# Optimization experiments

Hardware: AMD Instinct MI355X
Metric: run time of the kernel (lower is better)

The kernel has to match this reference:

```python
import jax, jax.numpy as jnp
import numpy as np

B, T, C = 4, 2048, 1024   # batch, seq_len, n_embd
H, D = 16, 64             # num heads, head dim (H*D == C)


def setup_inputs() -> dict:
    key = jax.random.key(0)
    ks = jax.random.split(key, 6)
    scale = 0.02
    x = jax.random.normal(ks[0], (B, T, C), dtype=jnp.float32)
    Wq = jax.random.normal(ks[1], (H, C, D), dtype=jnp.float32) * scale
    Wk = jax.random.normal(ks[2], (H, C, D), dtype=jnp.float32) * scale
    Wv = jax.random.normal(ks[3], (H, C, D), dtype=jnp.float32) * scale
    Wp = jax.random.normal(ks[4], (C, C), dtype=jnp.float32) * scale
    bp = jnp.zeros((C,), dtype=jnp.float32)
    return {"x": x, "Wq": Wq, "Wk": Wk, "Wv": Wv, "Wp": Wp, "bp": bp}


def reference(x, Wq, Wk, Wv, Wp, bp):
    # Batched per-head projections (equivalent to the per-head nn.Linear loop)
    q = jnp.einsum('btc,hcd->bhtd', x, Wq)
    k = jnp.einsum('btc,hcd->bhtd', x, Wk)
    v = jnp.einsum('btc,hcd->bhtd', x, Wv)
    # NOTE: original code scales by C**-0.5 where C = n_embd (not head dim)
    scores = jnp.einsum('bhtd,bhsd->bhts', q, k) * (C ** -0.5)
    causal = jnp.tril(jnp.ones((T, T), dtype=bool))  # [T, T]
    scores = jnp.where(causal, scores, -jnp.inf)
    att = jax.nn.softmax(scores, axis=-1)            # [B, H, T, T]
    out = jnp.einsum('bhts,bhsd->bhtd', att, v)      # [B, H, T, D]
    # concat heads (order matches torch.cat over head list) then output proj
    out = out.transpose(0, 2, 1, 3).reshape(B, T, H * D)
    return out @ Wp + bp
```

## Files before the change

### kernel.cpp

```cpp
#include <hip/hip_runtime.h>
#include <hip/hip_bf16.h>


#define B_ 4
#define T_ 2048
#define C_ 1024
#define H_ 16
#define D_ 64
#define M_ (B_*T_)

typedef unsigned short u16;
typedef unsigned short ushort4v __attribute__((ext_vector_type(4)));
typedef unsigned short ushort8 __attribute__((ext_vector_type(8)));
typedef unsigned int uint4v __attribute__((ext_vector_type(4)));
typedef int int2v __attribute__((ext_vector_type(2)));
typedef __attribute__((ext_vector_type(8))) short bf16x8;
typedef __attribute__((ext_vector_type(16))) float f32x16;

__device__ __forceinline__ u16 f2bf(float f) {
    __hip_bfloat16 h = __float2bfloat16(f);
    return *reinterpret_cast<u16*>(&h);
}
__device__ __forceinline__ unsigned pkt(float lo, float hi2) {
    return __builtin_amdgcn_perm(__float_as_uint(hi2), __float_as_uint(lo), 0x07060302u);
}
__device__ __forceinline__ void gload_lds16(const void* g, void* lds) {
    __builtin_amdgcn_global_load_lds((const __attribute__((address_space(1))) unsigned int*)g,
                                     (__attribute__((address_space(3))) unsigned int*)lds, 16, 0, 0);
}
__device__ __forceinline__ int swz4(int r) { return (r ^ (r >> 2)) & 3; }

__device__ __forceinline__ void ttile64(const float* __restrict__ in, int ldin,
                                        u16* __restrict__ out, int ldout, float scale) {
    __shared__ float t[64][65];
    const int tid = threadIdx.x;
    {
        int c = tid & 63, rr = tid >> 6;
        #pragma unroll
        for (int i = 0; i < 16; ++i) {
            int r = i * 4 + rr;
            t[r][c] = in[(size_t)r * ldin + c];
        }
    }
    __syncthreads();
    {
        int r2 = tid & 63, cg = tid >> 6;
        #pragma unroll
        for (int i = 0; i < 16; ++i) {
            int cc = i * 4 + cg;
            out[(size_t)cc * ldout + r2] = f2bf(t[r2][cc] * scale);
        }
    }
}

__global__ __launch_bounds__(256) void prep(const float* __restrict__ x,
                                            const float* __restrict__ Wq, const float* __restrict__ Wk,
                                            const float* __restrict__ Wv, const float* __restrict__ Wp,
                                            u16* __restrict__ xb, u16* __restrict__ Wt,
                                            u16* __restrict__ Wpt) {
    const int bid = blockIdx.x;
    if (bid < 4096) {
        int i = (bid * 256 + threadIdx.x) * 8;
        float4 a = *reinterpret_cast<const float4*>(x + i);
        float4 b = *reinterpret_cast<const float4*>(x + i + 4);
        ushort8 o;
        o[0]=f2bf(a.x); o[1]=f2bf(a.y); o[2]=f2bf(a.z); o[3]=f2bf(a.w);
        o[4]=f2bf(b.x); o[5]=f2bf(b.y); o[6]=f2bf(b.z); o[7]=f2bf(b.w);
        *reinterpret_cast<ushort8*>(xb + i) = o;
    } else if (bid < 4096 + 768) {
        int idx = bid - 4096;
        int r0 = (idx & 15) * 64, z = idx >> 4;
        int which = z >> 4, h = z & 15;
        const float* W = (which == 0 ? Wq : which == 1 ? Wk : Wv) + (size_t)h * C_ * D_;
        const float scale = (which == 0) ? 0.03125f * 1.4426950408889634f : 1.f;
        ttile64(W + (size_t)r0 * D_, D_, Wt + (size_t)(which * 16 + h) * 64 * C_ + r0, C_, scale);
    } else {
        int idx = bid - 4864;
        int r0 = (idx & 15) * 64, c0 = (idx >> 4) * 64;
        ttile64(Wp + (size_t)r0 * C_ + c0, C_, Wpt + (size_t)c0 * C_ + r0, C_, 1.f);
    }
}

__device__ __forceinline__ void gemm_core3(const u16* __restrict__ A, const u16* __restrict__ Bt,
                                           int m0, int n0, u16* lds, f32x16 (&acc)[4][2]) {
    const int tid = threadIdx.x;
    const int wid = tid >> 6, lane = tid & 63;
    const int l31 = lane & 31, hi = lane >> 5;
    const int wr = wid >> 1, wc = wid & 1;

    const u16* src[6];
    #pragma unroll
    for (int it = 0; it < 6; ++it) {
        int slot = it * 256 + tid;
        int row, g;
        const u16* base;
        if (it < 4) { row = slot >> 2; g = slot & 3; base = A + (size_t)(m0 + row) * C_; }
        else        { int s2 = slot - 1024; row = s2 >> 2; g = s2 & 3; base = Bt + (size_t)(n0 + row) * C_; }
        src[it] = base + ((g ^ swz4(row)) * 8);
    }

    const char* lb = reinterpret_cast<const char*>(lds);
    int aoff[2][4], boff[2][2];
    #pragma unroll
    for (int kk = 0; kk < 2; ++kk) {
        #pragma unroll
        for (int mt = 0; mt < 4; ++mt) {
            int row = wr * 128 + mt * 32 + l31;
            aoff[kk][mt] = row * 64 + (((kk * 2 + hi) ^ swz4(row)) & 3) * 16;
        }
        #pragma unroll
        for (int nt = 0; nt < 2; ++nt) {
            int row = wc * 64 + nt * 32 + l31;
            boff[kk][nt] = 16384 + row * 64 + (((kk * 2 + hi) ^ swz4(row)) & 3) * 16;
        }
    }

#define STG(BU16)                                                                   \
    {                                                                               \
        _Pragma("unroll")                                                           \
        for (int it = 0; it < 6; ++it) {                                            \
            gload_lds16(src[it], lds + (BU16) + (it * 256 + tid) * 8);              \
            src[it] += 32;                                                          \
        }                                                                           \
    }

    STG(0);
    STG(12288);

    #pragma unroll
    for (int t = 0; t < 32; ++t) {
        if (t < 31) { asm volatile("s_waitcnt vmcnt(6)" ::: "memory"); }
        else        { asm volatile("s_waitcnt vmcnt(0)" ::: "memory"); }
        __builtin_amdgcn_sched_barrier(0);
        __builtin_amdgcn_s_barrier();
        __builtin_amdgcn_sched_barrier(0);

        const char* lbuf = lb + (t & 1) * 24576;
        __builtin_amdgcn_s_setprio(1);
        #pragma unroll
        for (int kk = 0; kk < 2; ++kk) {
            bf16x8 bf0 = *reinterpret_cast<const bf16x8*>(lbuf + boff[kk][0]);
            bf16x8 bf1 = *reinterpret_cast<const bf16x8*>(lbuf + boff[kk][1]);
            #pragma unroll
            for (int mt = 0; mt < 4; ++mt) {
                bf16x8 af = *reinterpret_cast<const bf16x8*>(lbuf + aoff[kk][mt]);
                acc[mt][0] = __builtin_amdgcn_mfma_f32_32x32x16_bf16(af, bf0, acc[mt][0], 0, 0, 0);
                acc[mt][1] = __builtin_amdgcn_mfma_f32_32x32x16_bf16(af, bf1, acc[mt][1], 0, 0, 0);
            }
        }
        __builtin_amdgcn_s_setprio(0);
        __builtin_amdgcn_sched_barrier(0);
        __builtin_amdgcn_s_barrier();
        __builtin_amdgcn_sched_barrier(0);
        if (t + 2 < 32) STG((t & 1) * 12288);
    }
#undef STG
}

__global__ __launch_bounds__(256, 2) void qkv_gemm(const u16* __restrict__ xb, const u16* __restrict__ Wt,
                                                   u16* __restrict__ q, u16* __restrict__ k,
                                                   u16* __restrict__ vT) {
    __shared__ u16 lds[2 * 12288];
    f32x16 acc[4][2];
    #pragma unroll
    for (int i = 0; i < 4; ++i)
        #pragma unroll
        for (int j = 0; j < 2; ++j)
            #pragma unroll
            for (int r = 0; r < 16; ++r) acc[i][j][r] = 0.f;
    const int m0 = blockIdx.x * 256, n0 = blockIdx.y * 128;
    gemm_core3(xb, Wt, m0, n0, lds, acc);

    const int tid = threadIdx.x, wid = tid >> 6, lane = tid & 63;
    const int l31 = lane & 31, hi = lane >> 5;
    const int wr = wid >> 1, wc = wid & 1;
    #pragma unroll
    for (int mt = 0; mt < 4; ++mt) {
        #pragma unroll
        for (int nt = 0; nt < 2; ++nt) {
            int n = n0 + wc * 64 + nt * 32 + l31;
            int which = n >> 10, h = (n >> 6) & 15, d = n & 63;
            if (which < 2) {
                u16* dst = (which == 0 ? q : k);
                #pragma unroll
                for (int r = 0; r < 16; ++r) {
                    int m = m0 + wr * 128 + mt * 32 + (r & 3) + 8 * (r >> 2) + 4 * hi;
                    int b = m >> 11, t = m & (T_ - 1);
                    dst[((size_t)(b * H_ + h) * T_ + t) * D_ + d] = f2bf(acc[mt][nt][r]);
                }
            } else {
                #pragma unroll
                for (int rq = 0; rq < 4; ++rq) {
                    int m = m0 + wr * 128 + mt * 32 + 8 * rq + 4 * hi;
                    int b = m >> 11, t = m & (T_ - 1);
                    ushort4v pk;
                    pk[0] = f2bf(acc[mt][nt][rq * 4 + 0]);
                    pk[1] = f2bf(acc[mt][nt][rq * 4 + 1]);
                    pk[2] = f2bf(acc[mt][nt][rq * 4 + 2]);
                    pk[3] = f2bf(acc[mt][nt][rq * 4 + 3]);
                    *reinterpret_cast<ushort4v*>(
                        vT + ((size_t)(b * H_ + h) * D_ + d) * T_ + t) = pk;
                }
            }
        }
    }
}

__global__ __launch_bounds__(256, 2) void out_gemm(const u16* __restrict__ ob, const u16* __restrict__ Wpt,
                                                   const float* __restrict__ bp, float* __restrict__ out) {
    __shared__ u16 lds[2 * 12288];
    f32x16 acc[4][2];
    #pragma unroll
    for (int i = 0; i < 4; ++i)
        #pragma unroll
        for (int j = 0; j < 2; ++j)
            #pragma unroll
            for (int r = 0; r < 16; ++r) acc[i][j][r] = 0.f;
    const int m0 = blockIdx.x * 256, n0 = blockIdx.y * 128;
    gemm_core3(ob, Wpt, m0, n0, lds, acc);

    const int tid = threadIdx.x, wid = tid >> 6, lane = tid & 63;
    const int l31 = lane & 31, hi = lane >> 5;
    const int wr = wid >> 1, wc = wid & 1;
    #pragma unroll
    for (int mt = 0; mt < 4; ++mt) {
        #pragma unroll
        for (int nt = 0; nt < 2; ++nt) {
            int n = n0 + wc * 64 + nt * 32 + l31;
            float bv = bp[n];
            #pragma unroll
            for (int r = 0; r < 16; ++r) {
                int m = m0 + wr * 128 + mt * 32 + (r & 3) + 8 * (r >> 2) + 4 * hi;
                out[(size_t)m * C_ + n] = acc[mt][nt][r] + bv;
            }
        }
    }
}

template<int CUR>
__device__ __forceinline__ void attn_tile(const char* const (&pf)[4], const bf16x8 (&qf)[4],
                                          const f32x16& z16, float& lrun,
                                          f32x16& oacc0, f32x16& oacc1,
                                          bool isdiag, int relq, int hi) {
    f32x16 st0, st1;
    __builtin_amdgcn_s_setprio(1);
    {
        bf16x8 ka0 = *reinterpret_cast<const bf16x8*>(pf[0] + CUR * 32768);
        bf16x8 ka1 = *reinterpret_cast<const bf16x8*>(pf[0] + CUR * 32768 + 4096);
        st0 = __builtin_amdgcn_mfma_f32_32x32x16_bf16(ka0, qf[0], z16, 0, 0, 0);
        st1 = __builtin_amdgcn_mfma_f32_32x32x16_bf16(ka1, qf[0], z16, 0, 0, 0);
    }
    #pragma unroll
    for (int kc = 1; kc < 4; ++kc) {
        bf16x8 ka0 = *reinterpret_cast<const bf16x8*>(pf[kc] + CUR * 32768);
        bf16x8 ka1 = *reinterpret_cast<const bf16x8*>(pf[kc] + CUR * 32768 + 4096);
        st0 = __builtin_amdgcn_mfma_f32_32x32x16_bf16(ka0, qf[kc], st0, 0, 0, 0);
        st1 = __builtin_amdgcn_mfma_f32_32x32x16_bf16(ka1, qf[kc], st1, 0, 0, 0);
    }
    __builtin_amdgcn_s_setprio(0);

    if (isdiag) {
        #pragma unroll
        for (int rr = 0; rr < 16; ++rr) {
            int sl = (rr & 3) + 8 * (rr >> 2) + 4 * hi;
            if (sl > relq)      st0[rr] = -INFINITY;
            if (sl + 32 > relq) st1[rr] = -INFINITY;
        }
    }

    float rsum = 0.f;
    #pragma unroll
    for (int rr = 0; rr < 16; ++rr) {
        st0[rr] = __builtin_amdgcn_exp2f(st0[rr]);
        st1[rr] = __builtin_amdgcn_exp2f(st1[rr]);
        rsum += st0[rr] + st1[rr];
    }
    rsum += __shfl_xor(rsum, 32);
    lrun += rsum;

    bf16x8 pa0, pa1, pa2, pa3;
#if __has_builtin(__builtin_amdgcn_permlane32_swap)
#define MK_PA(PA, SV, RB)                                                          \
    {                                                                              \
        int X0 = (int)pkt(SV[RB + 0], SV[RB + 1]);                                 \
        int X1 = (int)pkt(SV[RB + 2], SV[RB + 3]);                                 \
        int Y0 = (int)pkt(SV[RB + 4], SV[RB + 5]);                                 \
        int Y1 = (int)pkt(SV[RB + 6], SV[RB + 7]);                                 \
        int2v r0 = __builtin_amdgcn_permlane32_swap(X0, Y0, false, false);         \
        int2v r1 = __builtin_amdgcn_permlane32_swap(X1, Y1, false, false);         \
        uint4v w; w[0] = (unsigned)r0[0]; w[1] = (unsigned)r1[0];                  \
        w[2] = (unsigned)r0[1]; w[3] = (unsigned)r1[1];                            \
        PA = __builtin_bit_cast(bf16x8, w);                                        \
    }
#else
#define MK_PA(PA, SV, RB)                                                          \
    {                                                                              \
        unsigned X0 = pkt(SV[RB + 0], SV[RB + 1]);                                 \
        unsigned X1 = pkt(SV[RB + 2], SV[RB + 3]);                                 \
        unsigned Y0 = pkt(SV[RB + 4], SV[RB + 5]);                                 \
        unsigned sX0 = __shfl_xor(X0, 32), sY0 = __shfl_xor(Y0, 32);               \
        unsigned Y1 = pkt(SV[RB + 6], SV[RB + 7]);                                 \
        unsigned sX1 = __shfl_xor(X1, 32), sY1 = __shfl_xor(Y1, 32);               \
        uint4v w;                                                                  \
        w[0] = hi ? sY0 : X0; w[1] = hi ? sY1 : X1;                                \
        w[2] = hi ? Y0 : sX0; w[3] = hi ? Y1 : sX1;                                \
        PA = __builtin_bit_cast(bf16x8, w);                                        \
    }
#endif
    MK_PA(pa0, st0, 0); MK_PA(pa1, st0, 8); MK_PA(pa2, st1, 0); MK_PA(pa3, st1, 8);
#undef MK_PA

    __builtin_amdgcn_s_setprio(1);
#define PV_STEP(SCJ, PAV)                                                          \
    {                                                                              \
        bf16x8 va0 = *reinterpret_cast<const bf16x8*>(pf[SCJ] + CUR * 32768 + 16384);        \
        bf16x8 va1 = *reinterpret_cast<const bf16x8*>(pf[SCJ] + CUR * 32768 + 16384 + 4096); \
        oacc0 = __builtin_amdgcn_mfma_f32_32x32x16_bf16(va0, PAV, oacc0, 0, 0, 0); \
        oacc1 = __builtin_amdgcn_mfma_f32_32x32x16_bf16(va1, PAV, oacc1, 0, 0, 0); \
    }
    PV_STEP(0, pa0) PV_STEP(1, pa1) PV_STEP(2, pa2) PV_STEP(3, pa3)
#undef PV_STEP
    __builtin_amdgcn_s_setprio(0);
}

__global__ __launch_bounds__(512, 4) void attn_mfma(const u16* __restrict__ q,
                                                    const u16* __restrict__ k,
                                                    const u16* __restrict__ vT,
                                                    u16* __restrict__ o) {
    __shared__ u16 smem[32768];

    const int tid  = threadIdx.x;
    const int wid  = tid >> 6;
    const int lane = tid & 63;
    const int l31  = lane & 31;
    const int hi   = lane >> 5;

    const int lin = blockIdx.x;
    const int xcd = lin & 7;
    const int i   = (lin >> 3) & 31;
    const int f   = lin >> 8;
    const int bh  = xcd * 8 + (i & 7);
    const int e   = i >> 3;
    const int qb  = f ? (7 - e) : e;

    const int q0 = qb * 256;
    const size_t base = (size_t)bh * T_ * D_;
    const u16* kp  = k  + base;
    const u16* vtp = vT + (size_t)bh * D_ * T_;
    const int qglob = q0 + wid * 32 + l31;

    bf16x8 qf[4];
    {
        const u16* qp = q + base + (size_t)qglob * D_;
        #pragma unroll
        for (int kc = 0; kc < 4; ++kc)
            qf[kc] = *reinterpret_cast<const bf16x8*>(qp + kc * 16 + hi * 8);
    }

    const int rw = tid >> 3;
    const int cg = (tid & 7) ^ (rw & 7);
    const u16* gK = kp  + (size_t)rw * D_ + cg * 8;
    const u16* gV = vtp + (size_t)rw * T_ + cg * 8;

    u16* sbase = &smem[0];
    u16* dK = sbase + tid * 8;
    u16* dV = sbase + 8192 + tid * 8;

    const char* pf[4];
    #pragma unroll
    for (int j = 0; j < 4; ++j)
        pf[j] = reinterpret_cast<const char*>(sbase) + l31 * 128 + (((j * 2 + hi) ^ (l31 & 7)) << 4);

    float lrun = 0.f;
    f32x16 oacc0, oacc1, z16;
    #pragma unroll
    for (int rr = 0; rr < 16; ++rr) { oacc0[rr] = 0.f; oacc1[rr] = 0.f; z16[rr] = 0.f; }

    const int ntile  = 4 * qb + 4;
    const int diag_t = 4 * qb + (wid >> 1);
    const int relq   = 32 * (wid & 1) + l31;

#define STG(BUFU16)                                                                \
    {                                                                              \
        gload_lds16(gK, dK + (BUFU16)); gload_lds16(gV, dV + (BUFU16));            \
        gK += 64 * D_; gV += 64;                                                   \
    }

    STG(0);
    __syncthreads();

    for (int tt = 0; tt < ntile; tt += 2) {
        if (tt + 1 < ntile) STG(16384);
        if (tt <= diag_t)
            attn_tile<0>(pf, qf, z16, lrun, oacc0, oacc1, tt == diag_t, relq, hi);
        __syncthreads();
        if (tt + 2 < ntile) STG(0);
        if (tt + 1 <= diag_t)
            attn_tile<1>(pf, qf, z16, lrun, oacc0, oacc1, tt + 1 == diag_t, relq, hi);
        __syncthreads();
    }
#undef STG

    float linv = 1.f / lrun;
    float* ot = reinterpret_cast<float*>(sbase) + wid * 2048;
    #pragma unroll
    for (int rr = 0; rr < 16; ++rr) {
        int d0v = (rr & 3) + 8 * (rr >> 2) + 4 * hi;
        int d1v = d0v + 32;
        ot[l31 * 64 + (((d0v >> 2) ^ (l31 & 7)) << 2) + (d0v & 3)] = oacc0[rr] * linv;
        ot[l31 * 64 + (((d1v >> 2) ^ (l31 & 7)) << 2) + (d1v & 3)] = oacc1[rr] * linv;
    }

    const int b = bh >> 4, h = bh & 15;
    const int qrow = lane >> 1;
    const int d0 = (lane & 1) * 32;
    u16 tmp[32];
    #pragma unroll
    for (int i2 = 0; i2 < 8; ++i2) {
        int g = ((d0 >> 2) + i2) ^ (qrow & 7);
        float4 fv = *reinterpret_cast<const float4*>(&ot[qrow * 64 + (g << 2)]);
        tmp[i2 * 4 + 0] = f2bf(fv.x); tmp[i2 * 4 + 1] = f2bf(fv.y);
        tmp[i2 * 4 + 2] = f2bf(fv.z); tmp[i2 * 4 + 3] = f2bf(fv.w);
    }
    u16* orow = o + ((size_t)b * T_ + q0 + wid * 32 + qrow) * C_ + h * 64 + d0;
    #pragma unroll
    for (int j = 0; j < 4; ++j)
        *reinterpret_cast<ushort8*>(orow + j * 8) = *reinterpret_cast<ushort8*>(&tmp[j * 8]);
}

extern "C" void kernel_launch(void* const* d_in, const int* in_sizes, int n_in,
                              void* d_out, int out_size, void* d_ws, size_t ws_size,
                              hipStream_t stream) {
    const float* x  = (const float*)d_in[0];
    const float* Wq = (const float*)d_in[1];
    const float* Wk = (const float*)d_in[2];
    const float* Wv = (const float*)d_in[3];
    const float* Wp = (const float*)d_in[4];
    const float* bp = (const float*)d_in[5];
    float* out = (float*)d_out;

    const size_t E = (size_t)M_ * C_;
    u16* xb  = (u16*)d_ws;
    u16* qb  = xb  + E;
    u16* kb  = qb  + E;
    u16* vTb = kb  + E;
    u16* obf = vTb + E;
    u16* Wt  = obf + E;
    u16* Wpt = Wt  + (size_t)3072 * 1024;

    prep<<<dim3(5120), 256, 0, stream>>>(x, Wq, Wk, Wv, Wp, xb, Wt, Wpt);

    qkv_gemm<<<dim3(M_ / 256, 3072 / 128), 256, 0, stream>>>(xb, Wt, qb, kb, vTb);

    attn_mfma<<<dim3(512), 512, 0, stream>>>(qb, kb, vTb, obf);

    out_gemm<<<dim3(M_ / 256, C_ / 128), 256, 0, stream>>>(obf, Wpt, bp, out);
}
```

Before: 141.6 us.

## Rework GEMM core to 8 waves with 16x16x32 MFMA and split-K slab pipeline

The QKV and output projection GEMMs move from 4 waves using 32x32x16 MFMAs to 8 waves per 256x128 tile using 16x16x32 MFMAs, with a 4x4 accumulator grid per wave. Each 64-wide K step is loaded as two 32-wide slabs into a larger double buffer, with loads issued between the two compute phases to deepen the prefetch. The epilogues are rewritten for the 16x16 output layout, and the V-transpose write keeps its 4-element packed stores. More waves can hide latency better, but the change adds an extra barrier per K step and needs a larger LDS footprint.

Measured after the change: 138.8 us. 2.0% less time.

```diff
diff --git a/kernel.cpp b/kernel.cpp
--- a/kernel.cpp
+++ b/kernel.cpp
@@ -15,6 +15,7 @@
 typedef unsigned int uint4v __attribute__((ext_vector_type(4)));
 typedef int int2v __attribute__((ext_vector_type(2)));
 typedef __attribute__((ext_vector_type(8))) short bf16x8;
+typedef __attribute__((ext_vector_type(4))) float f32x4;
 typedef __attribute__((ext_vector_type(16))) float f32x16;
 
 __device__ __forceinline__ u16 f2bf(float f) {
@@ -81,157 +82,156 @@
     }
 }
 
-__device__ __forceinline__ void gemm_core3(const u16* __restrict__ A, const u16* __restrict__ Bt,
-                                           int m0, int n0, u16* lds, f32x16 (&acc)[4][2]) {
+__device__ __forceinline__ void gemm_slab(const u16* __restrict__ A, const u16* __restrict__ Bt,
+                                          int m0, int n0, u16* lds, f32x4 (&acc)[4][4]) {
     const int tid = threadIdx.x;
     const int wid = tid >> 6, lane = tid & 63;
-    const int l31 = lane & 31, hi = lane >> 5;
-    const int wr = wid >> 1, wc = wid & 1;
-
-    const u16* src[6];
-    #pragma unroll
-    for (int it = 0; it < 6; ++it) {
-        int slot = it * 256 + tid;
-        int row, g;
-        const u16* base;
-        if (it < 4) { row = slot >> 2; g = slot & 3; base = A + (size_t)(m0 + row) * C_; }
-        else        { int s2 = slot - 1024; row = s2 >> 2; g = s2 & 3; base = Bt + (size_t)(n0 + row) * C_; }
-        src[it] = base + ((g ^ swz4(row)) * 8);
+    const int l16 = lane & 15, lq = lane >> 4;
+    const int wm = wid >> 1, wn = wid & 1;
+
+    const int rA0 = tid >> 2, rA1 = 128 + (tid >> 2), g0 = tid & 3;
+    const u16* pA0 = A  + (size_t)(m0 + rA0) * C_ + ((g0 ^ swz4(rA0)) * 8);
+    const u16* pA1 = A  + (size_t)(m0 + rA1) * C_ + ((g0 ^ swz4(rA1)) * 8);
+    const u16* pB0 = Bt + (size_t)(n0 + rA0) * C_ + ((g0 ^ swz4(rA0)) * 8);
+    const int dA0 = tid * 8, dA1 = 4096 + tid * 8, dB = 8192 + tid * 8;
+
+#define SLAB(T, CC)                                                                 \
+    {                                                                               \
+        const int bb = ((T) & 1) * 24576 + (CC) * 12288;                            \
+        const int ko = (T) * 64 + (CC) * 32;                                        \
+        gload_lds16(pA0 + ko, lds + bb + dA0);                                      \
+        gload_lds16(pA1 + ko, lds + bb + dA1);                                      \
+        gload_lds16(pB0 + ko, lds + bb + dB);                                       \
     }
 
     const char* lb = reinterpret_cast<const char*>(lds);
-    int aoff[2][4], boff[2][2];
-    #pragma unroll
-    for (int kk = 0; kk < 2; ++kk) {
-        #pragma unroll
-        for (int mt = 0; mt < 4; ++mt) {
-            int row = wr * 128 + mt * 32 + l31;
-            aoff[kk][mt] = row * 64 + (((kk * 2 + hi) ^ swz4(row)) & 3) * 16;
-        }
-        #pragma unroll
-        for (int nt = 0; nt < 2; ++nt) {
-            int row = wc * 64 + nt * 32 + l31;
-            boff[kk][nt] = 16384 + row * 64 + (((kk * 2 + hi) ^ swz4(row)) & 3) * 16;
-        }
-    }
-
-#define STG(BU16)                                                                   \
+    int aoff[4], boff[4];
+    #pragma unroll
+    for (int i = 0; i < 4; ++i) {
+        int ra = wm * 64 + i * 16 + l16;
+        aoff[i] = ra * 64 + ((lq ^ swz4(ra)) * 16);
+        int rb = wn * 64 + i * 16 + l16;
+        boff[i] = 16384 + rb * 64 + ((lq ^ swz4(rb)) * 16);
+    }
+
+#define PHASE(T, CC)                                                                \
     {                                                                               \
+        const char* sb = lb + (size_t)(((T) & 1) * 24576 + (CC) * 12288) * 2;       \
+        bf16x8 af[4], bfv[4];                                                       \
         _Pragma("unroll")                                                           \
-        for (int it = 0; it < 6; ++it) {                                            \
-            gload_lds16(src[it], lds + (BU16) + (it * 256 + tid) * 8);              \
-            src[it] += 32;                                                          \
+        for (int i = 0; i < 4; ++i) {                                               \
+            af[i]  = *reinterpret_cast<const bf16x8*>(sb + aoff[i]);                \
+            bfv[i] = *reinterpret_cast<const bf16x8*>(sb + boff[i]);                \
         }                                                                           \
-    }
-
-    STG(0);
-    STG(12288);
-
-    #pragma unroll
-    for (int t = 0; t < 32; ++t) {
-        if (t < 31) { asm volatile("s_waitcnt vmcnt(6)" ::: "memory"); }
+        __builtin_amdgcn_s_setprio(1);                                              \
+        _Pragma("unroll")                                                           \
+        for (int mt = 0; mt < 4; ++mt)                                              \
+            _Pragma("unroll")                                                       \
+            for (int nt = 0; nt < 4; ++nt)                                          \
+                acc[mt][nt] = __builtin_amdgcn_mfma_f32_16x16x32_bf16(               \
+                    af[mt], bfv[nt], acc[mt][nt], 0, 0, 0);                         \
+        __builtin_amdgcn_s_setprio(0);                                              \
+    }
+
+    SLAB(0, 0); SLAB(0, 1); SLAB(1, 0);
+
+    #pragma unroll
+    for (int t = 0; t < 16; ++t) {
+        if (t < 15) { asm volatile("s_waitcnt vmcnt(6)" ::: "memory"); }
+        else        { asm volatile("s_waitcnt vmcnt(3)" ::: "memory"); }
+        __builtin_amdgcn_sched_barrier(0);
+        __builtin_amdgcn_s_barrier();
+        __builtin_amdgcn_sched_barrier(0);
+        if (t + 1 < 16) SLAB(t + 1, 1);
+        PHASE(t, 0);
+        if (t < 15) { asm volatile("s_waitcnt vmcnt(6)" ::: "memory"); }
         else        { asm volatile("s_waitcnt vmcnt(0)" ::: "memory"); }
         __builtin_amdgcn_sched_barrier(0);
         __builtin_amdgcn_s_barrier();
         __builtin_amdgcn_sched_barrier(0);
-
-        const char* lbuf = lb + (t & 1) * 24576;
-        __builtin_amdgcn_s_setprio(1);
-        #pragma unroll
-        for (int kk = 0; kk < 2; ++kk) {
-            bf16x8 bf0 = *reinterpret_cast<const bf16x8*>(lbuf + boff[kk][0]);
-            bf16x8 bf1 = *reinterpret_cast<const bf16x8*>(lbuf + boff[kk][1]);
-            #pragma unroll
-            for (int mt = 0; mt < 4; ++mt) {
-                bf16x8 af = *reinterpret_cast<const bf16x8*>(lbuf + aoff[kk][mt]);
-                acc[mt][0] = __builtin_amdgcn_mfma_f32_32x32x16_bf16(af, bf0, acc[mt][0], 0, 0, 0);
-                acc[mt][1] = __builtin_amdgcn_mfma_f32_32x32x16_bf16(af, bf1, acc[mt][1], 0, 0, 0);
-            }
-        }
-        __builtin_amdgcn_s_setprio(0);
-        __builtin_amdgcn_sched_barrier(0);
-        __builtin_amdgcn_s_barrier();
-        __builtin_amdgcn_sched_barrier(0);
-        if (t + 2 < 32) STG((t & 1) * 12288);
-    }
-#undef STG
-}
-
-__global__ __launch_bounds__(256, 2) void qkv_gemm(const u16* __restrict__ xb, const u16* __restrict__ Wt,
+        if (t + 2 < 16) SLAB(t + 2, 0);
+        PHASE(t, 1);
+    }
+#undef SLAB
+#undef PHASE
+}
+
+__global__ __launch_bounds__(512, 2) void qkv_gemm(const u16* __restrict__ xb, const u16* __restrict__ Wt,
                                                    u16* __restrict__ q, u16* __restrict__ k,
                                                    u16* __restrict__ vT) {
-    __shared__ u16 lds[2 * 12288];
-    f32x16 acc[4][2];
+    __shared__ u16 lds[49152];
+    f32x4 acc[4][4];
     #pragma unroll
     for (int i = 0; i < 4; ++i)
         #pragma unroll
-        for (int j = 0; j < 2; ++j)
+        for (int j = 0; j < 4; ++j) { acc[i][j][0]=0.f; acc[i][j][1]=0.f; acc[i][j][2]=0.f; acc[i][j][3]=0.f; }
+    const int m0 = blockIdx.x * 256, n0 = blockIdx.y * 128;
+    gemm_slab(xb, Wt, m0, n0, lds, acc);
+
+    const int tid = threadIdx.x, wid = tid >> 6, lane = tid & 63;
+    const int l16 = lane & 15, lq = lane >> 4;
+    const int wm = wid >> 1, wn = wid & 1;
+    const int which = n0 >> 10;
+    if (which < 2) {
+        u16* dst0 = (which == 0 ? q : k);
+        #pragma unroll
+        for (int mt = 0; mt < 4; ++mt) {
             #pragma unroll
-            for (int r = 0; r < 16; ++r) acc[i][j][r] = 0.f;
-    const int m0 = blockIdx.x * 256, n0 = blockIdx.y * 128;
-    gemm_core3(xb, Wt, m0, n0, lds, acc);
-
-    const int tid = threadIdx.x, wid = tid >> 6, lane = tid & 63;
-    const int l31 = lane & 31, hi = lane >> 5;
-    const int wr = wid >> 1, wc = wid & 1;
-    #pragma unroll
-    for (int mt = 0; mt < 4; ++mt) {
-        #pragma unroll
-        for (int nt = 0; nt < 2; ++nt) {
-            int n = n0 + wc * 64 + nt * 32 + l31;
-            int which = n >> 10, h = (n >> 6) & 15, d = n & 63;
-            if (which < 2) {
-                u16* dst = (which == 0 ? q : k);
+            for (int j = 0; j < 4; ++j) {
+                int m = m0 + wm * 64 + mt * 16 + lq * 4 + j;
+                int b = m >> 11, t = m & (T_ - 1);
                 #pragma unroll
-                for (int r = 0; r < 16; ++r) {
-                    int m = m0 + wr * 128 + mt * 32 + (r & 3) + 8 * (r >> 2) + 4 * hi;
-                    int b = m >> 11, t = m & (T_ - 1);
-                    dst[((size_t)(b * H_ + h) * T_ + t) * D_ + d] = f2bf(acc[mt][nt][r]);
-                }
-            } else {
-                #pragma unroll
-                for (int rq = 0; rq < 4; ++rq) {
-                    int m = m0 + wr * 128 + mt * 32 + 8 * rq + 4 * hi;
-                    int b = m >> 11, t = m & (T_ - 1);
-                    ushort4v pk;
-                    pk[0] = f2bf(acc[mt][nt][rq * 4 + 0]);
-                    pk[1] = f2bf(acc[mt][nt][rq * 4 + 1]);
-                    pk[2] = f2bf(acc[mt][nt][rq * 4 + 2]);
-                    pk[3] = f2bf(acc[mt][nt][rq * 4 + 3]);
-                    *reinterpret_cast<ushort4v*>(
-                        vT + ((size_t)(b * H_ + h) * D_ + d) * T_ + t) = pk;
+                for (int nt = 0; nt < 4; ++nt) {
+                    int n = n0 + wn * 64 + nt * 16 + l16;
+                    int h = (n >> 6) & 15, d = n & 63;
+                    dst0[((size_t)(b * H_ + h) * T_ + t) * D_ + d] = f2bf(acc[mt][nt][j]);
                 }
             }
         }
-    }
-}
-
-__global__ __launch_bounds__(256, 2) void out_gemm(const u16* __restrict__ ob, const u16* __restrict__ Wpt,
+    } else {
+        #pragma unroll
+        for (int mt = 0; mt < 4; ++mt) {
+            int tb = m0 + wm * 64 + mt * 16 + lq * 4;
+            int b = tb >> 11, t = tb & (T_ - 1);
+            #pragma unroll
+            for (int nt = 0; nt < 4; ++nt) {
+                int n = n0 + wn * 64 + nt * 16 + l16;
+                int h = (n >> 6) & 15, d = n & 63;
+                ushort4v pk;
+                pk[0] = f2bf(acc[mt][nt][0]); pk[1] = f2bf(acc[mt][nt][1]);
+                pk[2] = f2bf(acc[mt][nt][2]); pk[3] = f2bf(acc[mt][nt][3]);
+                *reinterpret_cast<ushort4v*>(vT + ((size_t)(b * H_ + h) * D_ + d) * T_ + t) = pk;
+            }
+        }
+    }
+}
+
+__global__ __launch_bounds__(512, 2) void out_gemm(const u16* __restrict__ ob, const u16* __restrict__ Wpt,
                                                    const float* __restrict__ bp, float* __restrict__ out) {
-    __shared__ u16 lds[2 * 12288];
-    f32x16 acc[4][2];
+    __shared__ u16 lds[49152];
+    f32x4 acc[4][4];
     #pragma unroll
     for (int i = 0; i < 4; ++i)
         #pragma unroll
-        for (int j = 0; j < 2; ++j)
+        for (int j = 0; j < 4; ++j) { acc[i][j][0]=0.f; acc[i][j][1]=0.f; acc[i][j][2]=0.f; acc[i][j][3]=0.f; }
+    const int m0 = blockIdx.x * 256, n0 = blockIdx.y * 128;
+    gemm_slab(ob, Wpt, m0, n0, lds, acc);
+
+    const int tid = threadIdx.x, wid = tid >> 6, lane = tid & 63;
+    const int l16 = lane & 15, lq = lane >> 4;
+    const int wm = wid >> 1, wn = wid & 1;
+    float bv[4];
+    #pragma unroll
+    for (int nt = 0; nt < 4; ++nt) bv[nt] = bp[n0 + wn * 64 + nt * 16 + l16];
+    #pragma unroll
+    for (int mt = 0; mt < 4; ++mt) {
+        #pragma unroll
+        for (int j = 0; j < 4; ++j) {
+            int m = m0 + wm * 64 + mt * 16 + lq * 4 + j;
             #pragma unroll
-            for (int r = 0; r < 16; ++r) acc[i][j][r] = 0.f;
-    const int m0 = blockIdx.x * 256, n0 = blockIdx.y * 128;
-    gemm_core3(ob, Wpt, m0, n0, lds, acc);
-
-    const int tid = threadIdx.x, wid = tid >> 6, lane = tid & 63;
-    const int l31 = lane & 31, hi = lane >> 5;
-    const int wr = wid >> 1, wc = wid & 1;
-    #pragma unroll
-    for (int mt = 0; mt < 4; ++mt) {
-        #pragma unroll
-        for (int nt = 0; nt < 2; ++nt) {
-            int n = n0 + wc * 64 + nt * 32 + l31;
-            float bv = bp[n];
-            #pragma unroll
-            for (int r = 0; r < 16; ++r) {
-                int m = m0 + wr * 128 + mt * 32 + (r & 3) + 8 * (r >> 2) + 4 * hi;
-                out[(size_t)m * C_ + n] = acc[mt][nt][r] + bv;
+            for (int nt = 0; nt < 4; ++nt) {
+                int n = n0 + wn * 64 + nt * 16 + l16;
+                out[(size_t)m * C_ + n] = acc[mt][nt][j] + bv[nt];
             }
         }
     }
@@ -450,9 +450,9 @@
 
     prep<<<dim3(5120), 256, 0, stream>>>(x, Wq, Wk, Wv, Wp, xb, Wt, Wpt);
 
-    qkv_gemm<<<dim3(M_ / 256, 3072 / 128), 256, 0, stream>>>(xb, Wt, qb, kb, vTb);
+    qkv_gemm<<<dim3(M_ / 256, 3072 / 128), 512, 0, stream>>>(xb, Wt, qb, kb, vTb);
 
     attn_mfma<<<dim3(512), 512, 0, stream>>>(qb, kb, vTb, obf);
 
-    out_gemm<<<dim3(M_ / 256, C_ / 128), 256, 0, stream>>>(obf, Wpt, bp, out);
-}
+    out_gemm<<<dim3(M_ / 256, C_ / 128), 512, 0, stream>>>(obf, Wpt, bp, out);
+}
```
